# Optimization experiments

Measured on AMD Instinct MI355X. Metric: run time of the kernel, lower is better.

Reference implementation:

```python
import jax
import jax.numpy as jnp
from jax import lax
import numpy as np

N_LAYER = 8
SCALE = 4
H_CH = 128
Z_CH = 64


def conv2d(x, w, b=None, stride=1, pad=0):
    # x: NCHW, w: OIHW
    out = lax.conv_general_dilated(
        x, w, (stride, stride), [(pad, pad), (pad, pad)],
        dimension_numbers=("NCHW", "OIHW", "NCHW"))
    if b is not None:
        out = out + b[None, :, None, None]
    return out


def conv_transpose2d(x, w, stride):
    # torch ConvTranspose2d semantics, weight shape (in, out, kH, kW), no bias
    return lax.conv_transpose(
        x, w, (stride, stride), "VALID",
        dimension_numbers=("NCHW", "IOHW", "NCHW"), transpose_kernel=True)


def lstm_cell(inp, hidden, cell, gw, gb, tw, tb):
    # inp = inp + transform(hidden); gates fused into one conv (order f,i,o,s)
    inp = inp + conv2d(hidden, tw, tb, pad=2)
    gates = conv2d(inp, gw, gb, pad=2)
    f, i, o, s = jnp.split(gates, 4, axis=1)
    cell = jax.nn.sigmoid(f) * cell + jax.nn.sigmoid(i) * jnp.tanh(s)
    hidden = jax.nn.sigmoid(o) * jnp.tanh(cell)
    return hidden, cell


def setup_inputs() -> dict:
    key = jax.random.key(0)
    ks = jax.random.split(key, 24)
    b, xc, H, W = 64, 3, 64, 64
    vd, rd = 7, 256
    hs, ws = H // SCALE, W // SCALE
    enc_in = vd + rd + xc + H_CH   # 394
    dec_in = vd + rd + Z_CH        # 327

    def w_init(k, shape):
        fan_in = int(np.prod(shape[1:]))
        return jax.random.normal(k, shape, jnp.float32) / np.sqrt(fan_in)

    inp = {
        "x": jax.random.normal(ks[0], (b, xc, H, W), jnp.float32),
        "v": jax.random.normal(ks[1], (b, vd), jnp.float32),
        "r": jax.random.normal(ks[2], (b, rd, hs, ws), jnp.float32),
        "eps": jax.random.normal(ks[3], (N_LAYER, b, Z_CH, hs, ws), jnp.float32),
        "read_w": w_init(ks[4], (xc, xc, SCALE, SCALE)),
        "write_w": w_init(ks[5], (H_CH, H_CH, SCALE, SCALE)),  # (in,out,kH,kW)
        "prior_w": w_init(ks[6], (2 * Z_CH, H_CH, 5, 5)),
        "prior_b": jnp.zeros((2 * Z_CH,), jnp.float32),
        "post_w": w_init(ks[7], (2 * Z_CH, H_CH, 5, 5)),
        "post_b": jnp.zeros((2 * Z_CH,), jnp.float32),
        "enc_gw": w_init(ks[8], (4 * H_CH, enc_in, 5, 5)),
        "enc_gb": jnp.zeros((4 * H_CH,), jnp.float32),
        "enc_tw": w_init(ks[9], (enc_in, H_CH, 5, 5)),
        "enc_tb": jnp.zeros((enc_in,), jnp.float32),
        "dec_gw": w_init(ks[10], (4 * H_CH, dec_in, 5, 5)),
        "dec_gb": jnp.zeros((4 * H_CH,), jnp.float32),
        "dec_tw": w_init(ks[11], (dec_in, H_CH, 5, 5)),
        "dec_tb": jnp.zeros((dec_in,), jnp.float32),
        "obs_w": w_init(ks[12], (xc, H_CH, 1, 1)),
        "obs_b": jnp.zeros((xc,), jnp.float32),
    }
    return inp


def reference(x, v, r, eps, read_w, write_w, prior_w, prior_b, post_w, post_b,
              enc_gw, enc_gb, enc_tw, enc_tb, dec_gw, dec_gb, dec_tw, dec_tb,
              obs_w, obs_b):
    b, _, H, W = x.shape
    hs, ws = H // SCALE, W // SCALE
    dt = x.dtype
    h_enc = jnp.zeros((b, H_CH, hs, ws), dt)
    c_enc = jnp.zeros((b, H_CH, hs, ws), dt)
    h_dec = jnp.zeros((b, H_CH, hs, ws), dt)
    c_dec = jnp.zeros((b, H_CH, hs, ws), dt)
    u = jnp.zeros((b, H_CH, H, W), dt)

    xr = conv2d(x, read_w, stride=SCALE)            # (b, xc, hs, ws)
    vb = jnp.broadcast_to(v[:, :, None, None], (b, v.shape[1], hs, ws))
    rb = r if r.shape[2] == hs else jnp.tile(r, (1, 1, hs, ws))

    kl_loss = jnp.zeros((), dt)
    for t in range(N_LAYER):
        p_mu, p_lv = jnp.split(conv2d(h_dec, prior_w, prior_b, pad=2), 2, axis=1)
        h_enc, c_enc = lstm_cell(
            jnp.concatenate([h_dec, xr, vb, rb], axis=1),
            h_enc, c_enc, enc_gw, enc_gb, enc_tw, enc_tb)
        q_mu, q_lv = jnp.split(conv2d(h_enc, post_w, post_b, pad=2), 2, axis=1)
        z = q_mu + jnp.exp(0.5 * q_lv) * eps[t]
        h_dec, c_dec = lstm_cell(
            jnp.concatenate([z, vb, rb], axis=1),
            h_dec, c_dec, dec_gw, dec_gb, dec_tw, dec_tb)
        u = u + conv_transpose2d(h_dec, write_w, SCALE)
        # KL(q||p) with var = exp(logvar); log(var1/var0) = p_lv - q_lv
        kl = 0.5 * (jnp.exp(q_lv - p_lv)
                    + (p_mu - q_mu) ** 2 * jnp.exp(-p_lv)
                    - 1.0 + (p_lv - q_lv))
        kl_loss = kl_loss + kl.sum(axis=(1, 2, 3)).mean()

    canvas = jax.nn.sigmoid(conv2d(u, obs_w, obs_b))
    return canvas, kl_loss
```

## Files before the change

### kernel.cpp

```cpp
#include <hip/hip_runtime.h>
#include <hip/hip_bf16.h>

using bf16 = __hip_bfloat16;
typedef __attribute__((ext_vector_type(8))) short short8;
typedef __attribute__((ext_vector_type(4))) float f32x4;
typedef __attribute__((ext_vector_type(8))) int i32x8;
typedef __attribute__((ext_vector_type(4))) int i32x4;

#define DEVI __device__ __forceinline__

#define MTOT 16384
#define PADS 25600

DEVI float sigm_(float x){ return 1.f/(1.f+expf(-x)); }

DEVI long pidx_(int m){
  int nb = m>>8, iy=(m>>4)&15, ix=m&15;
  return (long)(nb*20 + iy + 2)*20 + (ix + 2);
}

DEVI unsigned char f2fp8(float x){
  int p = __builtin_amdgcn_cvt_pk_fp8_f32(x, 0.f, 0, false);
  return (unsigned char)(p & 0xFF);
}
DEVI float fp82f(unsigned char v){
  return __builtin_amdgcn_cvt_f32_fp8((int)v, 0);
}

DEVI void async16(const void* g, void* l) {
  __builtin_amdgcn_global_load_lds(
      (__attribute__((address_space(1))) void*)(unsigned long long)g,
      (__attribute__((address_space(3))) void*)(unsigned int)(unsigned long long)l,
      16, 0, 0);
}

template<int N> DEVI void waitbar(){
  if constexpr (N==0)      asm volatile("s_waitcnt vmcnt(0)\ns_barrier" ::: "memory");
  else if constexpr (N==3) asm volatile("s_waitcnt vmcnt(3)\ns_barrier" ::: "memory");
  else                     asm volatile("s_waitcnt vmcnt(6)\ns_barrier" ::: "memory");
}

template<int CA, int NS>
__global__ __launch_bounds__(256)
void conv_g8(const unsigned char* __restrict__ A8,
             const unsigned char* __restrict__ Bt8,
             const float* __restrict__ bias, bf16* __restrict__ outB)
{
  constexpr int Kp8 = NS*128;
  __shared__ alignas(16) unsigned char As[2][16384];
  __shared__ alignas(16) unsigned char Bs[2][16384];

  const int m0 = blockIdx.x<<7;
  const int n0 = blockIdx.y<<7;
  const int tid = threadIdx.x;
  const int wv = tid>>6, ln = tid&63;

  const int rr = tid>>3;
  const int lc = (tid&7) ^ (rr&7);
  long paRC[4], pbR[4];
  #pragma unroll
  for (int i=0;i<4;i++){
    int m = m0 + rr + (i<<5);
    paRC[i] = (long)(((m>>8)*20 + ((m>>4)&15))*20 + (m&15)) * CA;
    pbR[i]  = (long)(n0 + rr + (i<<5))*Kp8 + lc*16;
  }

  int cc = lc*16, tp = 0, ks = 0;
  auto stage = [&](int d){
    const int shiftC = ((tp/5)*20 + (tp%5)) * CA;
    char* la = (char*)&As[d][0] + (wv<<10);
    char* lb = (char*)&Bs[d][0] + (wv<<10);
    #pragma unroll
    for (int i=0;i<4;i++) async16(A8 + paRC[i] + shiftC + cc, la + i*4096);
    #pragma unroll
    for (int i=0;i<4;i++) async16(Bt8 + pbR[i] + ks, lb + i*4096);
    cc += 128; if (cc >= CA){ cc -= CA; tp++; }
    ks += 128;
  };

  f32x4 acc[4][4] = {};
  const int wm = wv>>1, wn = wv&1;
  const int rA0 = (wm<<6) + (ln&15);
  const int rB0 = (wn<<6) + (ln&15);
  const int xa = ln&7;
  const int q2 = (ln>>4)<<1;
  const int c0 = ((q2    ) ^ xa)<<4;
  const int c1 = ((q2 | 1) ^ xa)<<4;

  stage(0);
  for (int t=0; t<NS; ++t) {
    asm volatile("s_waitcnt vmcnt(0)\ns_barrier" ::: "memory");
    if (t+1 < NS) stage((t+1)&1);

    const char* as_ = (const char*)&As[t&1][0];
    const char* bs_ = (const char*)&Bs[t&1][0];
    i32x8 af[4], bfr[4];
    #pragma unroll
    for (int f=0; f<4; f++){
      const char* p = as_ + ((rA0 + (f<<4))<<7);
      ((i32x4*)&af[f])[0] = *(const i32x4*)(p + c0);
      ((i32x4*)&af[f])[1] = *(const i32x4*)(p + c1);
    }
    #pragma unroll
    for (int f=0; f<4; f++){
      const char* p = bs_ + ((rB0 + (f<<4))<<7);
      ((i32x4*)&bfr[f])[0] = *(const i32x4*)(p + c0);
      ((i32x4*)&bfr[f])[1] = *(const i32x4*)(p + c1);
    }
    __builtin_amdgcn_s_setprio(1);
    #pragma unroll
    for (int mf=0; mf<4; mf++)
      #pragma unroll
      for (int nf=0; nf<4; nf++)
        acc[mf][nf] = __builtin_amdgcn_mfma_scale_f32_16x16x128_f8f6f4(
            af[mf], bfr[nf], acc[mf][nf], 0, 0, 0, 127, 0, 122);
    __builtin_amdgcn_s_setprio(0);
  }

  const int mb = m0 + (wm<<6);
  const int nb = n0 + (wn<<6);
  const int ml = (ln>>4)<<2;
  const int nl = ln&15;
  #pragma unroll
  for (int mf=0; mf<4; mf++) {
    #pragma unroll
    for (int j=0; j<4; j++) {
      const int m = mb + (mf<<4) + ml + j;
      #pragma unroll
      for (int nf=0; nf<4; nf++) {
        const int n = nb + (nf<<4) + nl;
        outB[((long)m<<9) + n] = __float2bfloat16(acc[mf][nf][j] + bias[n]);
      }
    }
  }
}

template<int CA, int EPI>
DEVI void conv_body(const bf16* __restrict__ A, const bf16* __restrict__ Bt,
                    const float* __restrict__ bias, const float* __restrict__ bias2,
                    float* __restrict__ outF, bf16* __restrict__ outB,
                    unsigned char* __restrict__ out8,
                    const bf16* __restrict__ ST, const bf16* __restrict__ extra,
                    int s0, int s1, int m0, int n0,
                    bf16* AsBase, bf16* BsBase)
{
  constexpr int Kp = 25*CA;
  const int NS = s1 - s0;

  const int tid = threadIdx.x;
  const int wv = tid>>6, ln = tid&63;

  const int rA = tid>>2;
  const int qs = ((tid&3) ^ ((rA>>1)&3))<<3;
  const int mA0 = m0 + rA, mA1 = m0 + 128 + rA;
  const long paA0 = ((long)(((mA0>>8)*20 + ((mA0>>4)&15))*20 + (mA0&15)))*CA + qs;
  const long paA1 = ((long)(((mA1>>8)*20 + ((mA1>>4)&15))*20 + (mA1&15)))*CA + qs;
  const long pbB  = (long)(n0 + rA)*Kp + qs;

  int kk0 = s0*32;
  int c0 = kk0 % CA;
  int tap = kk0 / CA;
  int kh = tap/5, kw = tap%5;
  int ks = kk0;

  auto stage = [&](int d){
    const long sh = (long)(kh*20 + kw)*CA + c0;
    char* la = (char*)AsBase + d*16384 + (wv<<10);
    char* lb = (char*)BsBase + d*8192  + (wv<<10);
    async16(A + paA0 + sh, la);
    async16(A + paA1 + sh, la + 8192);
    async16(Bt + pbB + ks, lb);
    ks += 32;
    c0 += 32; if (c0==CA){ c0=0; if(++kw==5){kw=0; ++kh;} }
  };

  f32x4 acc[4][4] = {};
  const int wm = wv>>1, wn = wv&1;
  const int rowA = (wm<<6) + (ln&15);
  const int rowB = (wn<<6) + (ln&15);
  const int kqA = (((ln>>4) ^ ((rowA>>1)&3))<<4);
  const int kqB = (((ln>>4) ^ ((rowB>>1)&3))<<4);

  stage(0); stage(1);
  int bc = 0, bs = 2;
  for (int t=0; t<NS; ++t) {
    if (t+1 < NS) waitbar<3>();
    else          waitbar<0>();
    if (t+2 < NS) stage(bs);

    const char* as_ = (const char*)AsBase + bc*16384;
    const char* bs_ = (const char*)BsBase + bc*8192;
    short8 af[4], bfr[4];
    #pragma unroll
    for (int mf=0; mf<4; mf++)
      af[mf] = *(const short8*)(as_ + ((rowA + (mf<<4))<<6) + kqA);
    #pragma unroll
    for (int nf=0; nf<4; nf++)
      bfr[nf] = *(const short8*)(bs_ + ((rowB + (nf<<4))<<6) + kqB);
    __builtin_amdgcn_s_setprio(1);
    #pragma unroll
    for (int mf=0; mf<4; mf++)
      #pragma unroll
      for (int nf=0; nf<4; nf++)
        acc[mf][nf] = __builtin_amdgcn_mfma_f32_16x16x32_bf16(af[mf], bfr[nf], acc[mf][nf], 0,0,0);
    __builtin_amdgcn_s_setprio(0);
    bc = (bc==2)?0:bc+1; bs = (bs==2)?0:bs+1;
  }

  const int mb = m0 + (wm<<6);
  const int nb = n0 + (wn<<6);
  const int ml = (ln>>4)<<2;
  const int nl = ln&15;
  #pragma unroll
  for (int mf=0; mf<4; mf++) {
    #pragma unroll
    for (int j=0; j<4; j++) {
      const int m = mb + (mf<<4) + ml + j;
      const long pI = pidx_(m);
      #pragma unroll
      for (int nf=0; nf<4; nf++) {
        const int n = nb + (nf<<4) + nl;
        const float v = acc[mf][nf][j];
        if constexpr (EPI==2) {
          if (n < 416) {
            float b  = (n < 394) ? bias[n] : 0.f;
            float st = __bfloat162float(ST[(long)m*416 + n]);
            float e  = (n < 128) ? __bfloat162float(extra[(pI<<7) + n]) : 0.f;
            out8[pI*416 + n] = f2fp8(v + b + st + e);
          }
        } else if constexpr (EPI==4) {
          if (n < 352) {
            float b  = (n < 327) ? bias[n] : 0.f;
            float st = __bfloat162float(ST[(long)m*352 + n]);
            out8[pI*352 + n] = f2fp8(v + b + st);
          } else if (n >= 384) {
            outF[((long)m<<7) + (n-384)] = v + bias2[n-384];
          }
        } else {
          outB[((long)m<<7) + n] = __float2bfloat16(v);
        }
      }
    }
  }
}

__global__ __launch_bounds__(512)
void conv_tp(const bf16* __restrict__ hDec, const bf16* __restrict__ BtDP,
             const float* __restrict__ dec_tb, const float* __restrict__ prior_b,
             float* __restrict__ PriorO, unsigned char* __restrict__ sDec8,
             const bf16* __restrict__ STdec,
             const bf16* __restrict__ hEnc, const bf16* __restrict__ BtEncT,
             const float* __restrict__ enc_tb, unsigned char* __restrict__ sEnc8,
             const bf16* __restrict__ STenc,
             const float* __restrict__ Wc, float* __restrict__ uc)
{
  __shared__ alignas(16) bf16 As[3][256*32];
  __shared__ alignas(16) bf16 Bs[3][128*32];
  const int m0 = blockIdx.x<<8, n0 = blockIdx.y<<7;
  if (blockIdx.z == 0)
    conv_body<128,4>(hDec, BtDP, dec_tb, prior_b, PriorO, nullptr, sDec8,
                     STdec, nullptr, 0, 100, m0, n0, &As[0][0], &Bs[0][0]);
  else
    conv_body<128,2>(hEnc, BtEncT, enc_tb, nullptr, nullptr, nullptr, sEnc8,
                     STenc, hDec, 0, 100, m0, n0, &As[0][0], &Bs[0][0]);

  const int gid = blockIdx.z*256 + blockIdx.y*64 + blockIdx.x;
  const int tid = threadIdx.x;
  const int m = (gid<<5) + (tid>>4);
  const int pix = tid&15;
  const int nb = m>>8, iy=(m>>4)&15, ix=m&15;
  const bf16* __restrict__ h = hDec + (pidx_(m)<<7);
  float a0=0.f, a1=0.f, a2=0.f;
  #pragma unroll 4
  for (int c=0;c<128;c++) {
    float hv = __bfloat162float(h[c]);
    const float* wl = Wc + c*48 + pix*3;
    a0 += hv*wl[0]; a1 += hv*wl[1]; a2 += hv*wl[2];
  }
  const int ki = pix>>2, kj = pix&3;
  long ob = ((long)((nb<<6) + (iy<<2) + ki)*64 + (ix<<2) + kj)*3;
  uc[ob+0] += a0; uc[ob+1] += a1; uc[ob+2] += a2;
}

__global__ __launch_bounds__(512)
void conv_post(const bf16* __restrict__ hEnc, const bf16* __restrict__ BtPost,
               bf16* __restrict__ PP)
{
  __shared__ alignas(16) bf16 As[3][256*32];
  __shared__ alignas(16) bf16 Bs[3][128*32];
  const int z = blockIdx.z;
  conv_body<128,6>(hEnc, BtPost, nullptr, nullptr, nullptr,
                   PP + (long)z*MTOT*128, nullptr, nullptr, nullptr,
                   z*25, z*25+25, blockIdx.x<<8, 0, &As[0][0], &Bs[0][0]);
}

__global__ void repack_w_k(const float* __restrict__ w, bf16* __restrict__ Bt,
                           int O, int I, int CA, long total)
{
  long e = (long)blockIdx.x*256 + threadIdx.x;
  if (e >= total) return;
  const int Kp = 25*CA;
  int o = (int)(e / Kp);
  int k = (int)(e % Kp);
  int blk = k / CA, c = k % CA;
  float v = 0.f;
  if (o < O && c < I) v = w[((long)o*I + c)*25 + blk];
  Bt[e] = __float2bfloat16(v);
}

__global__ void repack_w8_k(const float* __restrict__ w, unsigned char* __restrict__ Bt,
                            int O, int I, int CA, int Kp8, long total)
{
  long e = (long)blockIdx.x*256 + threadIdx.x;
  if (e >= total) return;
  int o = (int)(e / Kp8);
  int k = (int)(e % Kp8);
  float v = 0.f;
  if (k < 25*CA) {
    int blk = k / CA, c = k % CA;
    if (o < O && c < I) v = w[((long)o*I + c)*25 + blk] * 32.0f;
  }
  Bt[e] = f2fp8(v);
}

__global__ void wcomb_k(const float* __restrict__ ww, const float* __restrict__ ow,
                        float* __restrict__ Wc)
{
  int idx = blockIdx.x*256 + threadIdx.x;
  if (idx >= 128*48) return;
  int c = idx / 48, rst = idx % 48;
  int pix = rst / 3, o = rst % 3;
  int ki = pix >> 2, kj = pix & 3;
  float a = 0.f;
  for (int mm=0; mm<128; mm++)
    a += ww[(((long)c*128 + mm)*4 + ki)*4 + kj] * ow[o*128 + mm];
  Wc[idx] = a;
}

__global__ void xr_k(const float* __restrict__ x, const float* __restrict__ rw,
                     float* __restrict__ xr)
{
  int idx = blockIdx.x*256 + threadIdx.x;
  if (idx >= MTOT*3) return;
  int m = idx / 3, o = idx % 3;
  int nb = m>>8, iy=(m>>4)&15, ix=m&15;
  float a = 0.f;
  for (int c=0;c<3;c++)
    for (int kh=0;kh<4;kh++)
      for (int kw=0;kw<4;kw++)
        a += x[((long)(nb*3+c)*64 + (iy*4+kh))*64 + (ix*4+kw)] * rw[((o*3+c)*4+kh)*4+kw];
  xr[idx] = a;
}

__global__ void st_enc_k(const float* __restrict__ xr, const float* __restrict__ v,
                         const float* __restrict__ r, bf16* __restrict__ ST)
{
  long g = (long)blockIdx.x*256 + threadIdx.x;
  if (g >= (long)MTOT*266) return;
  int m = (int)(g / 266), ch = (int)(g % 266);
  int nb = m>>8, sp = m&255;
  float val;
  if (ch < 3)       val = xr[m*3 + ch];
  else if (ch < 10) val = v[nb*7 + ch - 3];
  else              val = r[((long)nb*256 + (ch-10))*256 + sp];
  ST[(long)m*416 + 128 + ch] = __float2bfloat16(val);
}

__global__ void st_dec_k(const float* __restrict__ v, const float* __restrict__ r,
                         bf16* __restrict__ ST)
{
  long g = (long)blockIdx.x*256 + threadIdx.x;
  if (g >= (long)MTOT*263) return;
  int m = (int)(g / 263), ch = (int)(g % 263);
  int nb = m>>8, sp = m&255;
  float val;
  if (ch < 7) val = v[nb*7 + ch];
  else        val = r[((long)nb*256 + (ch-7))*256 + sp];
  ST[(long)m*352 + 64 + ch] = __float2bfloat16(val);
}

__global__ void lstm_k(const bf16* __restrict__ gates, float* __restrict__ cbuf,
                       bf16* __restrict__ hpad)
{
  int idx = blockIdx.x*256 + threadIdx.x;
  int m = idx >> 7, c = idx & 127;
  long gb = (long)m << 9;
  float f = __bfloat162float(gates[gb + c]);
  float i = __bfloat162float(gates[gb + 128 + c]);
  float o = __bfloat162float(gates[gb + 256 + c]);
  float s = __bfloat162float(gates[gb + 384 + c]);
  float cell = sigm_(f)*cbuf[idx] + sigm_(i)*tanhf(s);
  cbuf[idx] = cell;
  hpad[(pidx_(m)<<7) + c] = __float2bfloat16(sigm_(o)*tanhf(cell));
}

__global__ void zkl4_k(const bf16* __restrict__ PP, const float* __restrict__ pb,
                       const float* __restrict__ prior, const float* __restrict__ eps_t,
                       unsigned char* __restrict__ sDec8, float* __restrict__ part)
{
  __shared__ float wsum[4];
  const long PL = (long)MTOT*128;
  int idx = blockIdx.x*256 + threadIdx.x;
  int m = idx >> 6, c = idx & 63;
  float qm = pb[c], ql = pb[64 + c];
  #pragma unroll
  for (int z=0; z<4; ++z) {
    qm += __bfloat162float(PP[z*PL + ((long)m<<7) + c]);
    ql += __bfloat162float(PP[z*PL + ((long)m<<7) + 64 + c]);
  }
  long pbx = (long)m << 7;
  float pm = prior[pbx + c], pl = prior[pbx + 64 + c];
  int nb = m>>8, sp = m&255;
  float e = eps_t[((long)nb*64 + c)*256 + sp];
  float z = qm + expf(0.5f*ql)*e;
  long so = pidx_(m)*352 + c;
  sDec8[so] = f2fp8(fp82f(sDec8[so]) + z);
  float kl = expf(ql - pl) + (pm-qm)*(pm-qm)*expf(-pl) - 1.f + (pl - ql);
  #pragma unroll
  for (int off=32; off>0; off>>=1) kl += __shfl_down(kl, off);
  if ((threadIdx.x & 63) == 0) wsum[threadIdx.x >> 6] = kl;
  __syncthreads();
  if (threadIdx.x == 0)
    part[blockIdx.x] = wsum[0] + wsum[1] + wsum[2] + wsum[3];
}

__global__ __launch_bounds__(256)
void wrc_k(const bf16* __restrict__ hpad, const float* __restrict__ Wc,
           float* __restrict__ uc)
{
  __shared__ float Wl[128*48];
  for (int i = threadIdx.x; i < 128*48; i += 256) Wl[i] = Wc[i];
  __syncthreads();
  int t = threadIdx.x;
  int mloc = t >> 4, pix = t & 15;
  int m = (blockIdx.x<<4) + mloc;
  int nb = m>>8, iy=(m>>4)&15, ix=m&15;
  const bf16* h = hpad + (pidx_(m)<<7);
  float a0=0.f, a1=0.f, a2=0.f;
  for (int c=0;c<128;c++) {
    float hv = __bfloat162float(h[c]);
    const float* wl = Wl + c*48 + pix*3;
    a0 += hv*wl[0]; a1 += hv*wl[1]; a2 += hv*wl[2];
  }
  int ki = pix>>2, kj = pix&3;
  long ob = ((long)((nb<<6) + (iy<<2) + ki)*64 + (ix<<2) + kj)*3;
  uc[ob+0] += a0; uc[ob+1] += a1; uc[ob+2] += a2;
}

__global__ void canvas_k(const float* __restrict__ uc, const float* __restrict__ ob,
                         float* __restrict__ out)
{
  int idx = blockIdx.x*256 + threadIdx.x;
  int x = idx & 63, y = (idx>>6)&63;
  int rem = idx >> 12;
  int o = rem % 3, n = rem / 3;
  float v = uc[((long)((n<<6)+y)*64 + x)*3 + o] + ob[o];
  out[idx] = 1.f/(1.f+expf(-v));
}

__global__ void klred_k(const float* __restrict__ part, float* __restrict__ out)
{
  __shared__ float wsum[4];
  float a = 0.f;
  for (int i = threadIdx.x; i < 32768; i += 256) a += part[i];
  #pragma unroll
  for (int off=32; off>0; off>>=1) a += __shfl_down(a, off);
  if ((threadIdx.x & 63) == 0) wsum[threadIdx.x >> 6] = a;
  __syncthreads();
  if (threadIdx.x == 0)
    out[786432] = (wsum[0] + wsum[1] + wsum[2] + wsum[3]) * (0.5f/64.f);
}

static const long O_BT_POST  = 0;
static const long O_BT_ENCT  = O_BT_POST  + 819200;
static const long O_BT_DP    = O_BT_ENCT  + 3276800;
static const long O_BT_ENCG  = O_BT_DP    + 3276800;
static const long O_BT_DECG  = O_BT_ENCG  + 10649600;
static const long O_WCOMB    = O_BT_DECG  + 9011200;
static const long O_XR       = O_WCOMB    + 24576;
static const long O_KLP      = O_XR       + 196608;
static const long O_STENC    = O_KLP      + 131072;
static const long O_STDEC    = O_STENC    + 13631488;
static const long O_HENC     = O_STDEC    + 11534336;
static const long O_HDEC     = O_HENC     + 6553600;
static const long O_SENC     = O_HDEC     + 6553600;
static const long O_SDEC     = O_SENC     + 21299200;
static const long O_CENC     = O_SDEC     + 18022400;
static const long O_CDEC     = O_CENC     + 8388608;
static const long O_PRIOR    = O_CDEC     + 8388608;
static const long O_PG       = O_PRIOR    + 8388608;
static const long O_UC       = O_PG       + 33554432;
static const long WS_TOTAL   = O_UC       + 3145728;

extern "C" void kernel_launch(void* const* d_in, const int* in_sizes, int n_in,
                              void* d_out, int out_size, void* d_ws, size_t ws_size,
                              hipStream_t stream)
{
  const float* x       = (const float*)d_in[0];
  const float* v       = (const float*)d_in[1];
  const float* r       = (const float*)d_in[2];
  const float* eps     = (const float*)d_in[3];
  const float* read_w  = (const float*)d_in[4];
  const float* write_w = (const float*)d_in[5];
  const float* prior_w = (const float*)d_in[6];
  const float* prior_b = (const float*)d_in[7];
  const float* post_w  = (const float*)d_in[8];
  const float* post_b  = (const float*)d_in[9];
  const float* enc_gw  = (const float*)d_in[10];
  const float* enc_gb  = (const float*)d_in[11];
  const float* enc_tw  = (const float*)d_in[12];
  const float* enc_tb  = (const float*)d_in[13];
  const float* dec_gw  = (const float*)d_in[14];
  const float* dec_gb  = (const float*)d_in[15];
  const float* dec_tw  = (const float*)d_in[16];
  const float* dec_tb  = (const float*)d_in[17];
  const float* obs_w   = (const float*)d_in[18];
  const float* obs_b   = (const float*)d_in[19];

  char* ws = (char*)d_ws;
  bf16* BtPost  = (bf16*)(ws + O_BT_POST);
  bf16* BtEncT  = (bf16*)(ws + O_BT_ENCT);
  bf16* BtDP    = (bf16*)(ws + O_BT_DP);
  unsigned char* Bt8EncG = (unsigned char*)(ws + O_BT_ENCG);
  unsigned char* Bt8DecG = (unsigned char*)(ws + O_BT_DECG);
  float* Wcomb  = (float*)(ws + O_WCOMB);
  float* XR     = (float*)(ws + O_XR);
  float* KLpart = (float*)(ws + O_KLP);
  bf16* STenc   = (bf16*)(ws + O_STENC);
  bf16* STdec   = (bf16*)(ws + O_STDEC);
  bf16* hEnc    = (bf16*)(ws + O_HENC);
  bf16* hDec    = (bf16*)(ws + O_HDEC);
  unsigned char* sEnc8 = (unsigned char*)(ws + O_SENC);
  unsigned char* sDec8 = (unsigned char*)(ws + O_SDEC);
  float* cEnc   = (float*)(ws + O_CENC);
  float* cDec   = (float*)(ws + O_CDEC);
  float* PriorO = (float*)(ws + O_PRIOR);
  bf16* Gates   = (bf16*)(ws + O_PG);
  bf16* PostP   = (bf16*)(ws + O_PG + 16777216);
  float* Ucomb  = (float*)(ws + O_UC);
  float* out    = (float*)d_out;

  size_t clr = (size_t)WS_TOTAL; if (clr > ws_size) clr = ws_size;
  hipMemsetAsync(d_ws, 0, clr, stream);

  repack_w_k<<<1600, 256, 0, stream>>>(post_w,  BtPost, 128, 128, 128, 128L*3200);
  repack_w_k<<<6400, 256, 0, stream>>>(enc_tw,  BtEncT, 394, 128, 128, 512L*3200);
  repack_w_k<<<4800, 256, 0, stream>>>(dec_tw,  BtDP,   327, 128, 128, 384L*3200);
  repack_w_k<<<1600, 256, 0, stream>>>(prior_w, BtDP + 384L*3200, 128, 128, 128, 128L*3200);
  repack_w8_k<<<20992, 256, 0, stream>>>(enc_gw, Bt8EncG, 512, 394, 416, 82*128, 512L*10496);
  repack_w8_k<<<17664, 256, 0, stream>>>(dec_gw, Bt8DecG, 512, 327, 352, 69*128, 512L*8832);
  wcomb_k<<<24, 256, 0, stream>>>(write_w, obs_w, Wcomb);
  xr_k<<<192, 256, 0, stream>>>(x, read_w, XR);
  st_enc_k<<<(int)(((long)MTOT*266 + 255)/256), 256, 0, stream>>>(XR, v, r, STenc);
  st_dec_k<<<(int)(((long)MTOT*263 + 255)/256), 256, 0, stream>>>(v, r, STdec);

  for (int t = 0; t < 8; ++t) {
    conv_tp<<<dim3(64,4,2), 512, 0, stream>>>(
        hDec, BtDP, dec_tb, prior_b, PriorO, sDec8, STdec,
        hEnc, BtEncT, enc_tb, sEnc8, STenc, Wcomb, Ucomb);
    conv_g8<416,82><<<dim3(128,4), 256, 0, stream>>>(sEnc8, Bt8EncG, enc_gb, Gates);
    lstm_k<<<8192, 256, 0, stream>>>(Gates, cEnc, hEnc);
    conv_post<<<dim3(64,1,4), 512, 0, stream>>>(hEnc, BtPost, PostP);
    zkl4_k<<<4096, 256, 0, stream>>>(PostP, post_b, PriorO,
                                     eps + (long)t*64*64*256, sDec8,
                                     KLpart + (long)t*4096);
    conv_g8<352,69><<<dim3(128,4), 256, 0, stream>>>(sDec8, Bt8DecG, dec_gb, Gates);
    lstm_k<<<8192, 256, 0, stream>>>(Gates, cDec, hDec);
  }

  wrc_k<<<1024, 256, 0, stream>>>(hDec, Wcomb, Ucomb);
  canvas_k<<<3072, 256, 0, stream>>>(Ucomb, obs_b, out);
  klred_k<<<1, 256, 0, stream>>>(KLpart, out);
}
```

Measured before the change: 2.862 ms.

## Move transform and prior convolutions to FP8 MFMA via shared GEMM core

The hidden-state transform convolutions (encoder and decoder transform plus prior) now run on FP8 scaled MFMA through a shared g8_core, replacing the bf16 conv_body path. The LSTM kernel additionally writes an FP8 copy of the hidden state, and those weights are repacked to FP8. This halves operand bytes and uses the higher-throughput FP8 matrix instructions. The cost is lower precision in the recurrent transform path and an extra byte-wide store per hidden element.

```diff
diff --git a/kernel.cpp b/kernel.cpp
--- a/kernel.cpp
+++ b/kernel.cpp
@@ -41,17 +41,12 @@
 }
 
 template<int CA, int NS>
-__global__ __launch_bounds__(256)
-void conv_g8(const unsigned char* __restrict__ A8,
-             const unsigned char* __restrict__ Bt8,
-             const float* __restrict__ bias, bf16* __restrict__ outB)
+DEVI void g8_core(const unsigned char* __restrict__ A8,
+                  const unsigned char* __restrict__ Bt8,
+                  int m0, int n0, unsigned char* AsB, unsigned char* BsB,
+                  f32x4 (&acc)[4][4])
 {
   constexpr int Kp8 = NS*128;
-  __shared__ alignas(16) unsigned char As[2][16384];
-  __shared__ alignas(16) unsigned char Bs[2][16384];
-
-  const int m0 = blockIdx.x<<7;
-  const int n0 = blockIdx.y<<7;
   const int tid = threadIdx.x;
   const int wv = tid>>6, ln = tid&63;
 
@@ -68,8 +63,8 @@
   int cc = lc*16, tp = 0, ks = 0;
   auto stage = [&](int d){
     const int shiftC = ((tp/5)*20 + (tp%5)) * CA;
-    char* la = (char*)&As[d][0] + (wv<<10);
-    char* lb = (char*)&Bs[d][0] + (wv<<10);
+    char* la = (char*)AsB + d*16384 + (wv<<10);
+    char* lb = (char*)BsB + d*16384 + (wv<<10);
     #pragma unroll
     for (int i=0;i<4;i++) async16(A8 + paRC[i] + shiftC + cc, la + i*4096);
     #pragma unroll
@@ -78,7 +73,6 @@
     ks += 128;
   };
 
-  f32x4 acc[4][4] = {};
   const int wm = wv>>1, wn = wv&1;
   const int rA0 = (wm<<6) + (ln&15);
   const int rB0 = (wn<<6) + (ln&15);
@@ -92,8 +86,8 @@
     asm volatile("s_waitcnt vmcnt(0)\ns_barrier" ::: "memory");
     if (t+1 < NS) stage((t+1)&1);
 
-    const char* as_ = (const char*)&As[t&1][0];
-    const char* bs_ = (const char*)&Bs[t&1][0];
+    const char* as_ = (const char*)AsB + (t&1)*16384;
+    const char* bs_ = (const char*)BsB + (t&1)*16384;
     i32x8 af[4], bfr[4];
     #pragma unroll
     for (int f=0; f<4; f++){
@@ -116,13 +110,28 @@
             af[mf], bfr[nf], acc[mf][nf], 0, 0, 0, 127, 0, 122);
     __builtin_amdgcn_s_setprio(0);
   }
-
-  const int mb = m0 + (wm<<6);
-  const int nb = n0 + (wn<<6);
+}
+
+template<int CA, int NS>
+__global__ __launch_bounds__(256)
+void conv_g8(const unsigned char* __restrict__ A8,
+             const unsigned char* __restrict__ Bt8,
+             const float* __restrict__ bias, bf16* __restrict__ outB)
+{
+  __shared__ alignas(16) unsigned char As[2][16384];
+  __shared__ alignas(16) unsigned char Bs[2][16384];
+  const int m0 = blockIdx.x<<7, n0 = blockIdx.y<<7;
+  f32x4 acc[4][4] = {};
+  g8_core<CA,NS>(A8, Bt8, m0, n0, &As[0][0], &Bs[0][0], acc);
+
+  const int tid = threadIdx.x;
+  const int wv = tid>>6, ln = tid&63;
+  const int mb = m0 + ((wv>>1)<<6);
+  const int nb = n0 + ((wv&1)<<6);
   const int ml = (ln>>4)<<2;
   const int nl = ln&15;
   #pragma unroll
-  for (int mf=0; mf<4; mf++) {
+  for (int mf=0; mf<4; mf++)
     #pragma unroll
     for (int j=0; j<4; j++) {
       const int m = mb + (mf<<4) + ml + j;
@@ -132,15 +141,84 @@
         outB[((long)m<<9) + n] = __float2bfloat16(acc[mf][nf][j] + bias[n]);
       }
     }
-  }
+}
+
+__global__ __launch_bounds__(256)
+void conv_tp8(const unsigned char* __restrict__ h8Dec,
+              const unsigned char* __restrict__ h8Enc,
+              const unsigned char* __restrict__ Bt8DP,
+              const unsigned char* __restrict__ Bt8EncT,
+              const float* __restrict__ dec_tb, const float* __restrict__ prior_b,
+              const float* __restrict__ enc_tb,
+              float* __restrict__ PriorO,
+              unsigned char* __restrict__ sDec8, const bf16* __restrict__ STdec,
+              unsigned char* __restrict__ sEnc8, const bf16* __restrict__ STenc,
+              const bf16* __restrict__ hDecB,
+              const float* __restrict__ Wc, float* __restrict__ uc)
+{
+  __shared__ alignas(16) unsigned char As[2][16384];
+  __shared__ alignas(16) unsigned char Bs[2][16384];
+  const int z = blockIdx.z;
+  const int m0 = blockIdx.x<<7, n0 = blockIdx.y<<7;
+  f32x4 acc[4][4] = {};
+  if (z == 0) g8_core<128,25>(h8Dec, Bt8DP,   m0, n0, &As[0][0], &Bs[0][0], acc);
+  else        g8_core<128,25>(h8Enc, Bt8EncT, m0, n0, &As[0][0], &Bs[0][0], acc);
+
+  const int tid = threadIdx.x;
+  const int wv = tid>>6, ln = tid&63;
+  const int mb = m0 + ((wv>>1)<<6);
+  const int nb = n0 + ((wv&1)<<6);
+  const int ml = (ln>>4)<<2;
+  const int nl = ln&15;
+  #pragma unroll
+  for (int mf=0; mf<4; mf++)
+    #pragma unroll
+    for (int j=0; j<4; j++) {
+      const int m = mb + (mf<<4) + ml + j;
+      const long pI = pidx_(m);
+      #pragma unroll
+      for (int nf=0; nf<4; nf++) {
+        const int n = nb + (nf<<4) + nl;
+        const float v = acc[mf][nf][j];
+        if (z == 0) {
+          if (n < 352) {
+            float b  = (n < 327) ? dec_tb[n] : 0.f;
+            float st = __bfloat162float(STdec[(long)m*352 + n]);
+            sDec8[pI*352 + n] = f2fp8(v + b + st);
+          } else if (n >= 384) {
+            PriorO[((long)m<<7) + (n-384)] = v + prior_b[n-384];
+          }
+        } else {
+          if (n < 416) {
+            float b  = (n < 394) ? enc_tb[n] : 0.f;
+            float st = __bfloat162float(STenc[(long)m*416 + n]);
+            float e  = (n < 128) ? __bfloat162float(hDecB[(pI<<7) + n]) : 0.f;
+            sEnc8[pI*416 + n] = f2fp8(v + b + st + e);
+          }
+        }
+      }
+    }
+
+  const int gid = blockIdx.z*512 + blockIdx.y*128 + blockIdx.x;
+  const int m = (gid<<4) + (tid>>4);
+  const int pix = tid&15;
+  const int nb2 = m>>8, iy=(m>>4)&15, ix=m&15;
+  const bf16* __restrict__ h = hDecB + (pidx_(m)<<7);
+  float a0=0.f, a1=0.f, a2=0.f;
+  #pragma unroll 4
+  for (int c=0;c<128;c++) {
+    float hv = __bfloat162float(h[c]);
+    const float* wl = Wc + c*48 + pix*3;
+    a0 += hv*wl[0]; a1 += hv*wl[1]; a2 += hv*wl[2];
+  }
+  const int ki = pix>>2, kj = pix&3;
+  long ob = ((long)((nb2<<6) + (iy<<2) + ki)*64 + (ix<<2) + kj)*3;
+  uc[ob+0] += a0; uc[ob+1] += a1; uc[ob+2] += a2;
 }
 
 template<int CA, int EPI>
 DEVI void conv_body(const bf16* __restrict__ A, const bf16* __restrict__ Bt,
-                    const float* __restrict__ bias, const float* __restrict__ bias2,
-                    float* __restrict__ outF, bf16* __restrict__ outB,
-                    unsigned char* __restrict__ out8,
-                    const bf16* __restrict__ ST, const bf16* __restrict__ extra,
+                    bf16* __restrict__ outB,
                     int s0, int s1, int m0, int n0,
                     bf16* AsBase, bf16* BsBase)
 {
@@ -212,74 +290,16 @@
   const int ml = (ln>>4)<<2;
   const int nl = ln&15;
   #pragma unroll
-  for (int mf=0; mf<4; mf++) {
+  for (int mf=0; mf<4; mf++)
     #pragma unroll
     for (int j=0; j<4; j++) {
       const int m = mb + (mf<<4) + ml + j;
-      const long pI = pidx_(m);
       #pragma unroll
       for (int nf=0; nf<4; nf++) {
         const int n = nb + (nf<<4) + nl;
-        const float v = acc[mf][nf][j];
-        if constexpr (EPI==2) {
-          if (n < 416) {
-            float b  = (n < 394) ? bias[n] : 0.f;
-            float st = __bfloat162float(ST[(long)m*416 + n]);
-            float e  = (n < 128) ? __bfloat162float(extra[(pI<<7) + n]) : 0.f;
-            out8[pI*416 + n] = f2fp8(v + b + st + e);
-          }
-        } else if constexpr (EPI==4) {
-          if (n < 352) {
-            float b  = (n < 327) ? bias[n] : 0.f;
-            float st = __bfloat162float(ST[(long)m*352 + n]);
-            out8[pI*352 + n] = f2fp8(v + b + st);
-          } else if (n >= 384) {
-            outF[((long)m<<7) + (n-384)] = v + bias2[n-384];
-          }
-        } else {
-          outB[((long)m<<7) + n] = __float2bfloat16(v);
-        }
+        outB[((long)m<<7) + n] = __float2bfloat16(acc[mf][nf][j]);
       }
     }
-  }
-}
-
-__global__ __launch_bounds__(512)
-void conv_tp(const bf16* __restrict__ hDec, const bf16* __restrict__ BtDP,
-             const float* __restrict__ dec_tb, const float* __restrict__ prior_b,
-             float* __restrict__ PriorO, unsigned char* __restrict__ sDec8,
-             const bf16* __restrict__ STdec,
-             const bf16* __restrict__ hEnc, const bf16* __restrict__ BtEncT,
-             const float* __restrict__ enc_tb, unsigned char* __restrict__ sEnc8,
-             const bf16* __restrict__ STenc,
-             const float* __restrict__ Wc, float* __restrict__ uc)
-{
-  __shared__ alignas(16) bf16 As[3][256*32];
-  __shared__ alignas(16) bf16 Bs[3][128*32];
-  const int m0 = blockIdx.x<<8, n0 = blockIdx.y<<7;
-  if (blockIdx.z == 0)
-    conv_body<128,4>(hDec, BtDP, dec_tb, prior_b, PriorO, nullptr, sDec8,
-                     STdec, nullptr, 0, 100, m0, n0, &As[0][0], &Bs[0][0]);
-  else
-    conv_body<128,2>(hEnc, BtEncT, enc_tb, nullptr, nullptr, nullptr, sEnc8,
-                     STenc, hDec, 0, 100, m0, n0, &As[0][0], &Bs[0][0]);
-
-  const int gid = blockIdx.z*256 + blockIdx.y*64 + blockIdx.x;
-  const int tid = threadIdx.x;
-  const int m = (gid<<5) + (tid>>4);
-  const int pix = tid&15;
-  const int nb = m>>8, iy=(m>>4)&15, ix=m&15;
-  const bf16* __restrict__ h = hDec + (pidx_(m)<<7);
-  float a0=0.f, a1=0.f, a2=0.f;
-  #pragma unroll 4
-  for (int c=0;c<128;c++) {
-    float hv = __bfloat162float(h[c]);
-    const float* wl = Wc + c*48 + pix*3;
-    a0 += hv*wl[0]; a1 += hv*wl[1]; a2 += hv*wl[2];
-  }
-  const int ki = pix>>2, kj = pix&3;
-  long ob = ((long)((nb<<6) + (iy<<2) + ki)*64 + (ix<<2) + kj)*3;
-  uc[ob+0] += a0; uc[ob+1] += a1; uc[ob+2] += a2;
 }
 
 __global__ __launch_bounds__(512)
@@ -289,8 +309,7 @@
   __shared__ alignas(16) bf16 As[3][256*32];
   __shared__ alignas(16) bf16 Bs[3][128*32];
   const int z = blockIdx.z;
-  conv_body<128,6>(hEnc, BtPost, nullptr, nullptr, nullptr,
-                   PP + (long)z*MTOT*128, nullptr, nullptr, nullptr,
+  conv_body<128,6>(hEnc, BtPost, PP + (long)z*MTOT*128,
                    z*25, z*25+25, blockIdx.x<<8, 0, &As[0][0], &Bs[0][0]);
 }
 
@@ -380,7 +399,7 @@
 }
 
 __global__ void lstm_k(const bf16* __restrict__ gates, float* __restrict__ cbuf,
-                       bf16* __restrict__ hpad)
+                       bf16* __restrict__ hpad, unsigned char* __restrict__ h8)
 {
   int idx = blockIdx.x*256 + threadIdx.x;
   int m = idx >> 7, c = idx & 127;
@@ -391,7 +410,10 @@
   float s = __bfloat162float(gates[gb + 384 + c]);
   float cell = sigm_(f)*cbuf[idx] + sigm_(i)*tanhf(s);
   cbuf[idx] = cell;
-  hpad[(pidx_(m)<<7) + c] = __float2bfloat16(sigm_(o)*tanhf(cell));
+  float h = sigm_(o)*tanhf(cell);
+  long hp = (pidx_(m)<<7) + c;
+  hpad[hp] = __float2bfloat16(h);
+  h8[hp] = f2fp8(h);
 }
 
 __global__ void zkl4_k(const bf16* __restrict__ PP, const float* __restrict__ pb,
@@ -488,7 +510,9 @@
 static const long O_CENC     = O_SDEC     + 18022400;
 static const long O_CDEC     = O_CENC     + 8388608;
 static const long O_PRIOR    = O_CDEC     + 8388608;
-static const long O_PG       = O_PRIOR    + 8388608;
+static const long O_H8E      = O_PRIOR    + 8388608;
+static const long O_H8D      = O_H8E      + 3276800;
+static const long O_PG       = O_H8D      + 3276800;
 static const long O_UC       = O_PG       + 33554432;
 static const long WS_TOTAL   = O_UC       + 3145728;
 
@@ -519,8 +543,8 @@
 
   char* ws = (char*)d_ws;
   bf16* BtPost  = (bf16*)(ws + O_BT_POST);
-  bf16* BtEncT  = (bf16*)(ws + O_BT_ENCT);
-  bf16* BtDP    = (bf16*)(ws + O_BT_DP);
+  unsigned char* Bt8EncT = (unsigned char*)(ws + O_BT_ENCT);
+  unsigned char* Bt8DP   = (unsigned char*)(ws + O_BT_DP);
   unsigned char* Bt8EncG = (unsigned char*)(ws + O_BT_ENCG);
   unsigned char* Bt8DecG = (unsigned char*)(ws + O_BT_DECG);
   float* Wcomb  = (float*)(ws + O_WCOMB);
@@ -535,6 +559,8 @@
   float* cEnc   = (float*)(ws + O_CENC);
   float* cDec   = (float*)(ws + O_CDEC);
   float* PriorO = (float*)(ws + O_PRIOR);
+  unsigned char* h8Enc = (unsigned char*)(ws + O_H8E);
+  unsigned char* h8Dec = (unsigned char*)(ws + O_H8D);
   bf16* Gates   = (bf16*)(ws + O_PG);
   bf16* PostP   = (bf16*)(ws + O_PG + 16777216);
   float* Ucomb  = (float*)(ws + O_UC);
@@ -543,10 +569,10 @@
   size_t clr = (size_t)WS_TOTAL; if (clr > ws_size) clr = ws_size;
   hipMemsetAsync(d_ws, 0, clr, stream);
 
-  repack_w_k<<<1600, 256, 0, stream>>>(post_w,  BtPost, 128, 128, 128, 128L*3200);
-  repack_w_k<<<6400, 256, 0, stream>>>(enc_tw,  BtEncT, 394, 128, 128, 512L*3200);
-  repack_w_k<<<4800, 256, 0, stream>>>(dec_tw,  BtDP,   327, 128, 128, 384L*3200);
-  repack_w_k<<<1600, 256, 0, stream>>>(prior_w, BtDP + 384L*3200, 128, 128, 128, 128L*3200);
+  repack_w_k<<<1600, 256, 0, stream>>>(post_w, BtPost, 128, 128, 128, 128L*3200);
+  repack_w8_k<<<6400, 256, 0, stream>>>(enc_tw, Bt8EncT, 394, 128, 128, 3200, 512L*3200);
+  repack_w8_k<<<4800, 256, 0, stream>>>(dec_tw, Bt8DP, 327, 128, 128, 3200, 384L*3200);
+  repack_w8_k<<<1600, 256, 0, stream>>>(prior_w, Bt8DP + 384L*3200, 128, 128, 128, 3200, 128L*3200);
   repack_w8_k<<<20992, 256, 0, stream>>>(enc_gw, Bt8EncG, 512, 394, 416, 82*128, 512L*10496);
   repack_w8_k<<<17664, 256, 0, stream>>>(dec_gw, Bt8DecG, 512, 327, 352, 69*128, 512L*8832);
   wcomb_k<<<24, 256, 0, stream>>>(write_w, obs_w, Wcomb);
@@ -555,17 +581,17 @@
   st_dec_k<<<(int)(((long)MTOT*263 + 255)/256), 256, 0, stream>>>(v, r, STdec);
 
   for (int t = 0; t < 8; ++t) {
-    conv_tp<<<dim3(64,4,2), 512, 0, stream>>>(
-        hDec, BtDP, dec_tb, prior_b, PriorO, sDec8, STdec,
-        hEnc, BtEncT, enc_tb, sEnc8, STenc, Wcomb, Ucomb);
+    conv_tp8<<<dim3(128,4,2), 256, 0, stream>>>(
+        h8Dec, h8Enc, Bt8DP, Bt8EncT, dec_tb, prior_b, enc_tb,
+        PriorO, sDec8, STdec, sEnc8, STenc, hDec, Wcomb, Ucomb);
     conv_g8<416,82><<<dim3(128,4), 256, 0, stream>>>(sEnc8, Bt8EncG, enc_gb, Gates);
-    lstm_k<<<8192, 256, 0, stream>>>(Gates, cEnc, hEnc);
+    lstm_k<<<8192, 256, 0, stream>>>(Gates, cEnc, hEnc, h8Enc);
     conv_post<<<dim3(64,1,4), 512, 0, stream>>>(hEnc, BtPost, PostP);
     zkl4_k<<<4096, 256, 0, stream>>>(PostP, post_b, PriorO,
                                      eps + (long)t*64*64*256, sDec8,
                                      KLpart + (long)t*4096);
     conv_g8<352,69><<<dim3(128,4), 256, 0, stream>>>(sDec8, Bt8DecG, dec_gb, Gates);
-    lstm_k<<<8192, 256, 0, stream>>>(Gates, cDec, hDec);
+    lstm_k<<<8192, 256, 0, stream>>>(Gates, cDec, hDec, h8Dec);
   }
 
   wrc_k<<<1024, 256, 0, stream>>>(hDec, Wcomb, Ucomb);
```

New measurement: 2.685 ms. 1.07x faster.
